# Kernel tuning notes

Hardware: AMD Instinct MI355X
Metric: run time of the kernel (lower is better)

Reference implementation:

```python
import jax, jax.numpy as jnp
import numpy as np

B, T, C = 4, 2048, 768
H, D = 12, 64          # num_heads, head_size
R = 64                 # kv_lora_rank
ROPE_THETA = 10000.0


def setup_inputs() -> dict:
    key = jax.random.key(0)
    ks = jax.random.split(key, 8)
    s = lambda fan_in: 1.0 / np.sqrt(fan_in)
    return {
        "x":      jax.random.normal(ks[0], (B, T, C), jnp.float32),
        "Wq":     jax.random.normal(ks[1], (C, H * D), jnp.float32) * s(C),
        "Wdown":  jax.random.normal(ks[2], (C, R), jnp.float32) * s(C),
        "ln_g":   jnp.ones((R,), jnp.float32),
        "ln_b":   jnp.zeros((R,), jnp.float32),
        "Wup":    jax.random.normal(ks[3], (R, 2 * H * D), jnp.float32) * s(R),
        "Wo":     jax.random.normal(ks[4], (H * D, C), jnp.float32) * s(H * D),
        "bo":     jnp.zeros((C,), jnp.float32),
    }


def _rope_cos_sin(t, d, dtype):
    # freqs over half-dim, repeated twice (rotate-half convention)
    inv_freq = 1.0 / (ROPE_THETA ** (jnp.arange(0, d, 2, dtype=jnp.float32) / d))
    ang = jnp.arange(t, dtype=jnp.float32)[:, None] * inv_freq[None, :]  # [T, D/2]
    ang = jnp.concatenate([ang, ang], axis=-1)                            # [T, D]
    return jnp.cos(ang).astype(dtype), jnp.sin(ang).astype(dtype)


def _apply_rope(q, cos, sin):
    # q: [B, H, T, D]; cos/sin: [T, D]
    d2 = q.shape[-1] // 2
    rot = jnp.concatenate([-q[..., d2:], q[..., :d2]], axis=-1)
    return q * cos + rot * sin


def reference(x, Wq, Wdown, ln_g, ln_b, Wup, Wo, bo):
    b, t, c = x.shape
    q = (x @ Wq).reshape(b, t, H, D).transpose(0, 2, 1, 3)  # [B,H,T,D]

    ckv = x @ Wdown                                         # [B,T,R]
    mu = jnp.mean(ckv, axis=-1, keepdims=True)
    var = jnp.var(ckv, axis=-1, keepdims=True)
    ckv = (ckv - mu) * jax.lax.rsqrt(var + 1e-5) * ln_g + ln_b

    kv = (ckv @ Wup).reshape(b, t, 2, H, D)
    k = kv[:, :, 0].transpose(0, 2, 1, 3)                   # [B,H,T,D]
    v = kv[:, :, 1].transpose(0, 2, 1, 3)

    cos, sin = _rope_cos_sin(t, D, x.dtype)
    q = _apply_rope(q, cos, sin)
    k = _apply_rope(k, cos, sin)

    wei = jnp.einsum("bhqd,bhkd->bhqk", q, k) * (D ** -0.5)
    causal = jnp.tril(jnp.ones((t, t), bool))
    wei = jnp.where(causal, wei, -jnp.inf)
    wei = jax.nn.softmax(wei, axis=-1)                      # dropout: eval mode (identity)

    out = jnp.einsum("bhqk,bhkd->bhqd", wei, v)             # [B,H,T,D]
    out = out.transpose(0, 2, 1, 3).reshape(b, t, H * D)
    return out @ Wo + bo
```

## Files before the change

kernel.cpp:

```cpp
#include <hip/hip_runtime.h>
#include <hip/hip_bf16.h>
#include <math.h>

#define B_ 4
#define T_ 2048
#define C_ 768
#define H_ 12
#define D_ 64
#define R_ 64
#define BT_ (B_*T_)
#define HD_ (H_*D_)

typedef __attribute__((ext_vector_type(8))) short bf16x8;
typedef __attribute__((ext_vector_type(4))) float f32x4;

__device__ inline short f2bf(float f) {
  union { float f; unsigned u; } x; x.f = f;
  unsigned r = x.u + 0x7fffu + ((x.u >> 16) & 1u);
  return (short)(r >> 16);
}
__device__ inline float bf2f(short s) {
  union { unsigned u; float f; } x; x.u = ((unsigned)(unsigned short)s) << 16;
  return x.f;
}
__device__ inline unsigned pk_bf16(float a, float b) {
#if __has_builtin(__builtin_amdgcn_cvt_pk_bf16_f32)
  auto t = __builtin_amdgcn_cvt_pk_bf16_f32(a, b);
  unsigned u; __builtin_memcpy(&u, &t, sizeof(unsigned)); return u;
#else
  union { float f; unsigned u; } x, y; x.f = a; y.f = b;
  unsigned ra = (x.u + 0x7fffu + ((x.u >> 16) & 1u)) >> 16;
  unsigned rb = (y.u + 0x7fffu + ((y.u >> 16) & 1u)) & 0xffff0000u;
  return ra | rb;
#endif
}
__device__ inline float fexp2(float x) {
#if __has_builtin(__builtin_amdgcn_exp2f)
  return __builtin_amdgcn_exp2f(x);
#else
  return exp2f(x);
#endif
}
typedef __attribute__((address_space(3))) unsigned lds_u32;
typedef __attribute__((address_space(1))) const unsigned glb_u32;
__device__ inline void gload_lds16(const void* g, void* l) {
  __builtin_amdgcn_global_load_lds((glb_u32*)g, (lds_u32*)l, 16, 0, 0);
}

__global__ void convert_f32_bf16(const float* __restrict__ in, short* __restrict__ out, int n4) {
  int i = blockIdx.x * blockDim.x + threadIdx.x;
  if (i < n4) {
    float4 v = ((const float4*)in)[i];
    short4 o;
    o.x = f2bf(v.x); o.y = f2bf(v.y); o.z = f2bf(v.z); o.w = f2bf(v.w);
    ((short4*)out)[i] = o;
  }
}

__global__ void prep_all(const float* __restrict__ Wq, const float* __restrict__ Wd,
                         const float* __restrict__ Wup, const float* __restrict__ Wo,
                         short* __restrict__ W1T, short* __restrict__ WupT,
                         short* __restrict__ WoT,
                         float* __restrict__ cs, float* __restrict__ sn) {
  int idx = blockIdx.x * blockDim.x + threadIdx.x;
  const int S1 = 768*768, S2 = 64*768, S3 = 1536*64, S4 = 768*768, S5 = T_*32;
  if (idx < S1) {
    int n = idx / 768, k = idx - n*768;
    W1T[idx] = f2bf(Wq[(size_t)k*768 + n]);
  } else if (idx < S1+S2) {
    int i = idx - S1; int n = i / 768, k = i - n*768;
    W1T[idx] = f2bf(Wd[(size_t)k*64 + n]);
  } else if (idx < S1+S2+S3) {
    int i = idx - S1 - S2; int n = i / 64, k = i - n*64;
    WupT[i] = f2bf(Wup[(size_t)k*1536 + n]);
  } else if (idx < S1+S2+S3+S4) {
    int i = idx - S1 - S2 - S3; int n = i / 768, k = i - n*768;
    WoT[i] = f2bf(Wo[(size_t)k*768 + n]);
  } else if (idx < S1+S2+S3+S4+S5) {
    int i = idx - S1 - S2 - S3 - S4;
    int j = i & 31, t = i >> 5;
    float invf = exp2f(-(float)j * (13.287712379549449f / 32.f));
    float a = (float)t * invf;
    cs[i] = cosf(a);
    sn[i] = sinf(a);
  }
}

template<int MODE>
__global__ __launch_bounds__(256) void gemm128(
    const short* __restrict__ A, const short* __restrict__ Bt,
    int M, int N, int K, int NBvalid,
    float* __restrict__ out0, const float* __restrict__ bias,
    const float* __restrict__ bias2,
    short* __restrict__ ob0, short* __restrict__ ob1,
    const float* __restrict__ cs, const float* __restrict__ sn)
{
  __shared__ short As[128 * 64];
  __shared__ short Bs[128 * 64];
  const int m0 = blockIdx.x * 128;
  const int n0 = blockIdx.y * 128;
  const int tid = threadIdx.x, lane = tid & 63, w = tid >> 6;
  const int wr = w >> 1, wc = w & 1;
  const int fr = lane & 15, fk = (lane >> 4) * 8;
  const int rstage = lane >> 3;
  const int cstage = (lane & 7) * 8;

  f32x4 acc[4][4] = {};

  for (int k0 = 0; k0 < K; k0 += 64) {
    __syncthreads();
    #pragma unroll
    for (int i = 0; i < 4; ++i) {
      int c = w * 4 + i;
      int r = c * 8 + rstage;
      gload_lds16(&A[(size_t)(m0 + r) * K + k0 + cstage], &As[c * 512]);
      if (n0 + c * 8 < NBvalid)
        gload_lds16(&Bt[(size_t)(n0 + r) * K + k0 + cstage], &Bs[c * 512]);
    }
    __syncthreads();
    #pragma unroll
    for (int kk = 0; kk < 64; kk += 32) {
      bf16x8 a[4], b[4];
      #pragma unroll
      for (int i = 0; i < 4; ++i) {
        a[i] = *(const bf16x8*)&As[(wr * 64 + i * 16 + fr) * 64 + kk + fk];
        b[i] = *(const bf16x8*)&Bs[(wc * 64 + i * 16 + fr) * 64 + kk + fk];
      }
      #pragma unroll
      for (int mi = 0; mi < 4; ++mi)
        #pragma unroll
        for (int ni = 0; ni < 4; ++ni)
          acc[mi][ni] = __builtin_amdgcn_mfma_f32_16x16x32_bf16(a[mi], b[ni], acc[mi][ni], 0, 0, 0);
    }
  }

  const int er = (lane >> 4) * 4, ec = lane & 15;
  const int colbase = n0 + wc * 64;

  if constexpr (MODE == 2) {
    #pragma unroll
    for (int mi = 0; mi < 4; ++mi)
      #pragma unroll
      for (int r = 0; r < 4; ++r) {
        int row = m0 + wr * 64 + mi * 16 + er + r;
        #pragma unroll
        for (int ni = 0; ni < 4; ++ni) {
          int col = colbase + ni * 16 + ec;
          out0[(size_t)row * N + col] = acc[mi][ni][r] + bias[col];
        }
      }
    return;
  }

  if constexpr (MODE == 0) {
    if (colbase < 768) {
      int h = colbase >> 6;
      #pragma unroll
      for (int mi = 0; mi < 4; ++mi)
        #pragma unroll
        for (int r = 0; r < 4; ++r) {
          int row = m0 + wr * 64 + mi * 16 + er + r;
          int t = row & (T_ - 1), bb = row >> 11;
          short* dst = ob0 + (((size_t)(bb * H_ + h)) * T_ + t) * 64;
          #pragma unroll
          for (int ni = 0; ni < 2; ++ni) {
            int d = ni * 16 + ec;
            float c = cs[t * 32 + d], s = sn[t * 32 + d];
            float x0 = acc[mi][ni][r], x1 = acc[mi][ni + 2][r];
            dst[d]      = f2bf(x0 * c - x1 * s);
            dst[d + 32] = f2bf(x1 * c + x0 * s);
          }
        }
    } else if (colbase < 832) {
      #pragma unroll
      for (int mi = 0; mi < 4; ++mi)
        #pragma unroll
        for (int r = 0; r < 4; ++r) {
          float s = 0.f, s2 = 0.f;
          #pragma unroll
          for (int ni = 0; ni < 4; ++ni) { float v = acc[mi][ni][r]; s += v; s2 += v*v; }
          #pragma unroll
          for (int off = 1; off < 16; off <<= 1) {
            s  += __shfl_xor(s, off);
            s2 += __shfl_xor(s2, off);
          }
          float mu = s * (1.f/64.f);
          float var = s2 * (1.f/64.f) - mu * mu;
          float rstd = rsqrtf(var + 1e-5f);
          int row = m0 + wr * 64 + mi * 16 + er + r;
          #pragma unroll
          for (int ni = 0; ni < 4; ++ni) {
            int d = ni * 16 + ec;
            ob1[(size_t)row * 64 + d] = f2bf((acc[mi][ni][r] - mu) * rstd * bias[d] + bias2[d]);
          }
        }
    }
  } else {
    if (colbase < 768) {
      int h = colbase >> 6;
      #pragma unroll
      for (int mi = 0; mi < 4; ++mi)
        #pragma unroll
        for (int r = 0; r < 4; ++r) {
          int row = m0 + wr * 64 + mi * 16 + er + r;
          int t = row & (T_ - 1), bb = row >> 11;
          short* dst = ob0 + (((size_t)(bb * H_ + h)) * T_ + t) * 64;
          #pragma unroll
          for (int ni = 0; ni < 2; ++ni) {
            int d = ni * 16 + ec;
            float c = cs[t * 32 + d], s = sn[t * 32 + d];
            float x0 = acc[mi][ni][r], x1 = acc[mi][ni + 2][r];
            dst[d]      = f2bf(x0 * c - x1 * s);
            dst[d + 32] = f2bf(x1 * c + x0 * s);
          }
        }
    } else {
      __syncthreads();
      short* Wl = (w < 2) ? &As[w * 4096] : &Bs[(w - 2) * 4096];
      int h = (colbase - 768) >> 6;
      #pragma unroll
      for (int mi = 0; mi < 4; ++mi) {
        int tl0 = mi * 16 + er;
        #pragma unroll
        for (int ni = 0; ni < 4; ++ni) {
          int d = ni * 16 + ec;
          int col = (tl0 + (d & 7) * 8) & 63;
          uint2 uu;
          uu.x = pk_bf16(acc[mi][ni][0], acc[mi][ni][1]);
          uu.y = pk_bf16(acc[mi][ni][2], acc[mi][ni][3]);
          *(uint2*)&Wl[d * 64 + col] = uu;
        }
      }
      __syncthreads();
      int bb = m0 >> 11;
      int tg0 = (m0 & (T_ - 1)) + wr * 64;
      int dlow = lane >> 3, tc = lane & 7;
      #pragma unroll
      for (int j = 0; j < 8; ++j) {
        int d = j * 8 + dlow;
        int col = (tc * 8 + (d & 7) * 8) & 63;
        uint4 vv = *(const uint4*)&Wl[d * 64 + col];
        *(uint4*)&ob1[((size_t)(bb * H_ + h) * 64 + d) * T_ + tg0 + tc * 8] = vv;
      }
    }
  }
}

#define SC2_ 0.18033688f

__global__ __launch_bounds__(256) void attn_mfma(
    const short* __restrict__ qgl, const short* __restrict__ kg,
    const short* __restrict__ vtg, short* __restrict__ o)
{
  __shared__ short Ks[8 * 512];
  __shared__ short Vts[8 * 512];
  __shared__ short Ps[4 * 16 * 72];

  const int bh = blockIdx.x;
  const int tid = threadIdx.x, lane = tid & 63, w = tid >> 6;
  const int q16 = lane & 15, quad = lane >> 4;
  short* Pw = &Ps[w * 16 * 72];
  const short* kb  = kg  + (size_t)bh * T_ * 64;
  const short* vtb = vtg + (size_t)bh * 64 * T_;
  const int b = bh / H_, h = bh - b * H_;

  #pragma unroll
  for (int phase = 0; phase < 2; ++phase) {
    const int qt = phase == 0 ? (31 - (int)blockIdx.y) : (int)blockIdx.y;
    const int q0 = qt * 64 + w * 16;
    const int qidx = q0 + q16;

    const short* qrow = qgl + ((size_t)bh * T_ + qidx) * 64;
    bf16x8 bq0 = *(const bf16x8*)&qrow[quad * 8];
    bf16x8 bq1 = *(const bf16x8*)&qrow[32 + quad * 8];

    f32x4 oacc[4] = {};
    float lrun = 0.f;
    const int qlast = qt * 64;

    for (int kt = 0; kt <= qlast; kt += 64) {
      __syncthreads();
      #pragma unroll
      for (int i = 0; i < 2; ++i) {
        int c = w * 2 + i;
        int s = c >> 1, ch = c & 1;
        gload_lds16(kb  + (size_t)(kt + s * 16 + q16) * 64 + ch * 32 + quad * 8, &Ks[c * 512]);
        gload_lds16(vtb + (size_t)(s * 16 + q16) * T_ + kt + ch * 32 + quad * 8, &Vts[c * 512]);
      }
      __syncthreads();

      f32x4 sacc[4];
      #pragma unroll
      for (int s = 0; s < 4; ++s) {
        bf16x8 a0 = *(const bf16x8*)&Ks[(s * 2 + 0) * 512 + lane * 8];
        bf16x8 a1 = *(const bf16x8*)&Ks[(s * 2 + 1) * 512 + lane * 8];
        f32x4 t0 = {};
        t0 = __builtin_amdgcn_mfma_f32_16x16x32_bf16(a0, bq0, t0, 0, 0, 0);
        t0 = __builtin_amdgcn_mfma_f32_16x16x32_bf16(a1, bq1, t0, 0, 0, 0);
        sacc[s] = t0;
      }

      float pv[16];
      float ls = 0.f;
      if (kt != qlast) {
        #pragma unroll
        for (int s = 0; s < 4; ++s)
          #pragma unroll
          for (int r = 0; r < 4; ++r) {
            float p = fexp2(sacc[s][r] * SC2_);
            pv[s * 4 + r] = p; ls += p;
          }
      } else {
        #pragma unroll
        for (int s = 0; s < 4; ++s)
          #pragma unroll
          for (int r = 0; r < 4; ++r) {
            int key = kt + s * 16 + quad * 4 + r;
            float p = (key <= qidx) ? fexp2(sacc[s][r] * SC2_) : 0.f;
            pv[s * 4 + r] = p; ls += p;
          }
      }
      ls += __shfl_xor(ls, 16);
      ls += __shfl_xor(ls, 32);
      lrun += ls;

      #pragma unroll
      for (int s = 0; s < 4; ++s) {
        uint2 uu;
        uu.x = pk_bf16(pv[s * 4 + 0], pv[s * 4 + 1]);
        uu.y = pk_bf16(pv[s * 4 + 2], pv[s * 4 + 3]);
        *(uint2*)&Pw[q16 * 72 + s * 16 + quad * 4] = uu;
      }

      #pragma unroll
      for (int c = 0; c < 2; ++c) {
        bf16x8 bp = *(const bf16x8*)&Pw[q16 * 72 + c * 32 + quad * 8];
        #pragma unroll
        for (int ms = 0; ms < 4; ++ms) {
          bf16x8 av = *(const bf16x8*)&Vts[(ms * 2 + c) * 512 + lane * 8];
          oacc[ms] = __builtin_amdgcn_mfma_f32_16x16x32_bf16(av, bp, oacc[ms], 0, 0, 0);
        }
      }
    }

    float inv = 1.f / lrun;
    #pragma unroll
    for (int ms = 0; ms < 4; ++ms) {
      uint2 uu;
      uu.x = pk_bf16(oacc[ms][0] * inv, oacc[ms][1] * inv);
      uu.y = pk_bf16(oacc[ms][2] * inv, oacc[ms][3] * inv);
      *(uint2*)&Pw[q16 * 72 + ms * 16 + quad * 4] = uu;
    }
    int row = lane >> 2, cc2 = (lane & 3) * 16;
    uint4 r0 = *(const uint4*)&Pw[row * 72 + cc2];
    uint4 r1 = *(const uint4*)&Pw[row * 72 + cc2 + 8];
    int t = q0 + row;
    short* orow = o + ((size_t)(b * T_ + t)) * HD_ + h * 64 + cc2;
    *(uint4*)&orow[0] = r0;
    *(uint4*)&orow[8] = r1;
  }
}

extern "C" void kernel_launch(void* const* d_in, const int* in_sizes, int n_in,
                              void* d_out, int out_size, void* d_ws, size_t ws_size,
                              hipStream_t stream) {
  (void)in_sizes; (void)n_in; (void)out_size; (void)ws_size;
  const float* x     = (const float*)d_in[0];
  const float* Wq    = (const float*)d_in[1];
  const float* Wdown = (const float*)d_in[2];
  const float* ln_g  = (const float*)d_in[3];
  const float* ln_b  = (const float*)d_in[4];
  const float* Wup   = (const float*)d_in[5];
  const float* Wo    = (const float*)d_in[6];
  const float* bo    = (const float*)d_in[7];
  float* out = (float*)d_out;

  char* w = (char*)d_ws;
  short* x_bf   = (short*)w;  w += (size_t)BT_ * C_    * 2;
  short* W1T    = (short*)w;  w += (size_t)832 * C_    * 2;
  short* WupT   = (short*)w;  w += (size_t)2*HD_ * R_  * 2;
  short* WoT    = (short*)w;  w += (size_t)HD_ * C_    * 2;
  short* ckv    = (short*)w;  w += (size_t)BT_ * R_    * 2;
  short* qb     = (short*)w;  w += (size_t)BT_ * HD_   * 2;
  short* kb     = (short*)w;  w += (size_t)BT_ * HD_   * 2;
  short* vt     = (short*)w;  w += (size_t)BT_ * HD_   * 2;
  short* att    = (short*)w;  w += (size_t)BT_ * HD_   * 2;
  float* cs_t   = (float*)w;  w += (size_t)T_ * 32 * 4;
  float* sn_t   = (float*)w;  w += (size_t)T_ * 32 * 4;

  {
    const int tot = 768*768 + 64*768 + 1536*64 + 768*768 + T_*32;
    prep_all<<<(tot + 255)/256, 256, 0, stream>>>(Wq, Wdown, Wup, Wo, W1T, WupT, WoT, cs_t, sn_t);
  }
  convert_f32_bf16<<<(BT_*C_/4 + 255)/256, 256, 0, stream>>>(x, x_bf, BT_*C_/4);

  gemm128<0><<<dim3(BT_/128, 7), 256, 0, stream>>>(
      x_bf, W1T, BT_, 896, C_, 832, nullptr, ln_g, ln_b, qb, ckv, cs_t, sn_t);

  gemm128<1><<<dim3(BT_/128, 12), 256, 0, stream>>>(
      ckv, WupT, BT_, 2*HD_, R_, 2*HD_, nullptr, nullptr, nullptr, kb, vt, cs_t, sn_t);

  attn_mfma<<<dim3(B_*H_, 16), 256, 0, stream>>>(qb, kb, vt, att);

  gemm128<2><<<dim3(BT_/128, 6), 256, 0, stream>>>(
      att, WoT, BT_, C_, HD_, C_, out, bo, nullptr, nullptr, nullptr, nullptr, nullptr);
}
```

Baseline: 207.2 us.

## Share K/V tiles across paired query tiles with double-buffered loads; tile weight transposes

The attention kernel now processes both paired query tiles (long and short causal rows) in one pass over the key tiles. Each K/V tile is loaded once and reused for both, and the next tile is prefetched into a second LDS buffer while the current one is computed. The softmax scale is folded into the RoPE cos/sin applied to q, which removes a multiply per score. The weight-prep kernel now transposes through a padded shared-memory tile so global reads and writes are coalesced. The costs are doubled LDS for K/V and more accumulator registers, which may reduce occupancy.

```diff
diff --git a/kernel.cpp b/kernel.cpp
--- a/kernel.cpp
+++ b/kernel.cpp
@@ -57,34 +57,52 @@
   }
 }
 
-__global__ void prep_all(const float* __restrict__ Wq, const float* __restrict__ Wd,
-                         const float* __restrict__ Wup, const float* __restrict__ Wo,
-                         short* __restrict__ W1T, short* __restrict__ WupT,
-                         short* __restrict__ WoT,
-                         float* __restrict__ cs, float* __restrict__ sn) {
-  int idx = blockIdx.x * blockDim.x + threadIdx.x;
-  const int S1 = 768*768, S2 = 64*768, S3 = 1536*64, S4 = 768*768, S5 = T_*32;
-  if (idx < S1) {
-    int n = idx / 768, k = idx - n*768;
-    W1T[idx] = f2bf(Wq[(size_t)k*768 + n]);
-  } else if (idx < S1+S2) {
-    int i = idx - S1; int n = i / 768, k = i - n*768;
-    W1T[idx] = f2bf(Wd[(size_t)k*64 + n]);
-  } else if (idx < S1+S2+S3) {
-    int i = idx - S1 - S2; int n = i / 64, k = i - n*64;
-    WupT[i] = f2bf(Wup[(size_t)k*1536 + n]);
-  } else if (idx < S1+S2+S3+S4) {
-    int i = idx - S1 - S2 - S3; int n = i / 768, k = i - n*768;
-    WoT[i] = f2bf(Wo[(size_t)k*768 + n]);
-  } else if (idx < S1+S2+S3+S4+S5) {
-    int i = idx - S1 - S2 - S3 - S4;
-    int j = i & 31, t = i >> 5;
-    float invf = exp2f(-(float)j * (13.287712379549449f / 32.f));
-    float a = (float)t * invf;
-    cs[i] = cosf(a);
-    sn[i] = sinf(a);
-  }
-}
+__device__ inline void ttile(const float* __restrict__ src, short* __restrict__ dst,
+                             int K, int N, int k0, int n0, int tid, float (*tl)[33]) {
+  int tx = tid & 31, ty = tid >> 5;
+  #pragma unroll
+  for (int r = 0; r < 4; ++r)
+    tl[ty + 8 * r][tx] = src[(size_t)(k0 + ty + 8 * r) * N + n0 + tx];
+  __syncthreads();
+  #pragma unroll
+  for (int r = 0; r < 4; ++r)
+    dst[(size_t)(n0 + ty + 8 * r) * K + k0 + tx] = f2bf(tl[tx][ty + 8 * r]);
+}
+
+__global__ __launch_bounds__(256) void prep_all(
+    const float* __restrict__ Wq, const float* __restrict__ Wd,
+    const float* __restrict__ Wup, const float* __restrict__ Wo,
+    short* __restrict__ W1T, short* __restrict__ WupT, short* __restrict__ WoT,
+    float* __restrict__ cs, float* __restrict__ sn) {
+  __shared__ float tl[32][33];
+  int blk = blockIdx.x, tid = threadIdx.x;
+  if (blk < 576) {
+    int tk = blk % 24, tn = blk / 24;
+    ttile(Wq, W1T, 768, 768, tk * 32, tn * 32, tid, tl);
+  } else if (blk < 624) {
+    int l = blk - 576; int tk = l % 24, tn = l / 24;
+    ttile(Wd, W1T + (size_t)768 * 768, 768, 64, tk * 32, tn * 32, tid, tl);
+  } else if (blk < 720) {
+    int l = blk - 624; int tk = l % 2, tn = l / 2;
+    ttile(Wup, WupT, 64, 1536, tk * 32, tn * 32, tid, tl);
+  } else if (blk < 1296) {
+    int l = blk - 720; int tk = l % 24, tn = l / 24;
+    ttile(Wo, WoT, 768, 768, tk * 32, tn * 32, tid, tl);
+  } else {
+    int base = (blk - 1296) * 1024;
+    #pragma unroll
+    for (int i = 0; i < 4; ++i) {
+      int idx = base + tid + i * 256;
+      int j = idx & 31, t = idx >> 5;
+      float invf = exp2f(-(float)j * (13.287712379549449f / 32.f));
+      float a = (float)t * invf;
+      cs[idx] = cosf(a);
+      sn[idx] = sinf(a);
+    }
+  }
+}
+
+#define SC2_ 0.18033688f
 
 template<int MODE>
 __global__ __launch_bounds__(256) void gemm128(
@@ -165,7 +183,7 @@
           #pragma unroll
           for (int ni = 0; ni < 2; ++ni) {
             int d = ni * 16 + ec;
-            float c = cs[t * 32 + d], s = sn[t * 32 + d];
+            float c = cs[t * 32 + d] * SC2_, s = sn[t * 32 + d] * SC2_;
             float x0 = acc[mi][ni][r], x1 = acc[mi][ni + 2][r];
             dst[d]      = f2bf(x0 * c - x1 * s);
             dst[d + 32] = f2bf(x1 * c + x0 * s);
@@ -246,17 +264,17 @@
   }
 }
 
-#define SC2_ 0.18033688f
-
 __global__ __launch_bounds__(256) void attn_mfma(
     const short* __restrict__ qgl, const short* __restrict__ kg,
     const short* __restrict__ vtg, short* __restrict__ o)
 {
-  __shared__ short Ks[8 * 512];
-  __shared__ short Vts[8 * 512];
+  __shared__ short Ks[2][4096];
+  __shared__ short Vts[2][4096];
   __shared__ short Ps[4 * 16 * 72];
 
   const int bh = blockIdx.x;
+  const int y  = blockIdx.y;
+  const int qt1 = 31 - y, qt2 = y;
   const int tid = threadIdx.x, lane = tid & 63, w = tid >> 6;
   const int q16 = lane & 15, quad = lane >> 4;
   short* Pw = &Ps[w * 16 * 72];
@@ -264,50 +282,61 @@
   const short* vtb = vtg + (size_t)bh * 64 * T_;
   const int b = bh / H_, h = bh - b * H_;
 
+  const int qbase[2] = {qt1 * 64 + w * 16, qt2 * 64 + w * 16};
+  bf16x8 bq[2][2];
   #pragma unroll
-  for (int phase = 0; phase < 2; ++phase) {
-    const int qt = phase == 0 ? (31 - (int)blockIdx.y) : (int)blockIdx.y;
-    const int q0 = qt * 64 + w * 16;
-    const int qidx = q0 + q16;
-
-    const short* qrow = qgl + ((size_t)bh * T_ + qidx) * 64;
-    bf16x8 bq0 = *(const bf16x8*)&qrow[quad * 8];
-    bf16x8 bq1 = *(const bf16x8*)&qrow[32 + quad * 8];
-
-    f32x4 oacc[4] = {};
-    float lrun = 0.f;
-    const int qlast = qt * 64;
-
-    for (int kt = 0; kt <= qlast; kt += 64) {
-      __syncthreads();
-      #pragma unroll
-      for (int i = 0; i < 2; ++i) {
-        int c = w * 2 + i;
-        int s = c >> 1, ch = c & 1;
-        gload_lds16(kb  + (size_t)(kt + s * 16 + q16) * 64 + ch * 32 + quad * 8, &Ks[c * 512]);
-        gload_lds16(vtb + (size_t)(s * 16 + q16) * T_ + kt + ch * 32 + quad * 8, &Vts[c * 512]);
-      }
-      __syncthreads();
+  for (int g = 0; g < 2; ++g) {
+    const short* qrow = qgl + ((size_t)bh * T_ + qbase[g] + q16) * 64;
+    bq[g][0] = *(const bf16x8*)&qrow[quad * 8];
+    bq[g][1] = *(const bf16x8*)&qrow[32 + quad * 8];
+  }
+
+  f32x4 oacc[2][4] = {};
+  float lrun[2] = {0.f, 0.f};
+  const int last  = qt1 * 64;
+  const int last2 = qt2 * 64;
+
+  auto stage = [&](int kt, int ib) {
+    #pragma unroll
+    for (int i = 0; i < 2; ++i) {
+      int c = w * 2 + i;
+      int s = c >> 1, ch = c & 1;
+      gload_lds16(kb  + (size_t)(kt + s * 16 + q16) * 64 + ch * 32 + quad * 8, &Ks[ib][c * 512]);
+      gload_lds16(vtb + (size_t)(s * 16 + q16) * T_ + kt + ch * 32 + quad * 8, &Vts[ib][c * 512]);
+    }
+  };
+
+  stage(0, 0);
+  int ib = 0;
+  for (int kt = 0; kt <= last; kt += 64, ib ^= 1) {
+    __syncthreads();
+    if (kt + 64 <= last) stage(kt + 64, ib ^ 1);
+
+    #pragma unroll
+    for (int g = 0; g < 2; ++g) {
+      if (g == 1 && kt > last2) break;
+      const int diag_end = (g == 0) ? last : last2;
+      const int qidx = qbase[g] + q16;
 
       f32x4 sacc[4];
       #pragma unroll
       for (int s = 0; s < 4; ++s) {
-        bf16x8 a0 = *(const bf16x8*)&Ks[(s * 2 + 0) * 512 + lane * 8];
-        bf16x8 a1 = *(const bf16x8*)&Ks[(s * 2 + 1) * 512 + lane * 8];
+        bf16x8 a0 = *(const bf16x8*)&Ks[ib][(s * 2 + 0) * 512 + lane * 8];
+        bf16x8 a1 = *(const bf16x8*)&Ks[ib][(s * 2 + 1) * 512 + lane * 8];
         f32x4 t0 = {};
-        t0 = __builtin_amdgcn_mfma_f32_16x16x32_bf16(a0, bq0, t0, 0, 0, 0);
-        t0 = __builtin_amdgcn_mfma_f32_16x16x32_bf16(a1, bq1, t0, 0, 0, 0);
+        t0 = __builtin_amdgcn_mfma_f32_16x16x32_bf16(a0, bq[g][0], t0, 0, 0, 0);
+        t0 = __builtin_amdgcn_mfma_f32_16x16x32_bf16(a1, bq[g][1], t0, 0, 0, 0);
         sacc[s] = t0;
       }
 
       float pv[16];
       float ls = 0.f;
-      if (kt != qlast) {
+      if (kt != diag_end) {
         #pragma unroll
         for (int s = 0; s < 4; ++s)
           #pragma unroll
           for (int r = 0; r < 4; ++r) {
-            float p = fexp2(sacc[s][r] * SC2_);
+            float p = fexp2(sacc[s][r]);
             pv[s * 4 + r] = p; ls += p;
           }
       } else {
@@ -316,13 +345,13 @@
           #pragma unroll
           for (int r = 0; r < 4; ++r) {
             int key = kt + s * 16 + quad * 4 + r;
-            float p = (key <= qidx) ? fexp2(sacc[s][r] * SC2_) : 0.f;
+            float p = (key <= qidx) ? fexp2(sacc[s][r]) : 0.f;
             pv[s * 4 + r] = p; ls += p;
           }
       }
       ls += __shfl_xor(ls, 16);
       ls += __shfl_xor(ls, 32);
-      lrun += ls;
+      lrun[g] += ls;
 
       #pragma unroll
       for (int s = 0; s < 4; ++s) {
@@ -337,24 +366,27 @@
         bf16x8 bp = *(const bf16x8*)&Pw[q16 * 72 + c * 32 + quad * 8];
         #pragma unroll
         for (int ms = 0; ms < 4; ++ms) {
-          bf16x8 av = *(const bf16x8*)&Vts[(ms * 2 + c) * 512 + lane * 8];
-          oacc[ms] = __builtin_amdgcn_mfma_f32_16x16x32_bf16(av, bp, oacc[ms], 0, 0, 0);
-        }
-      }
-    }
-
-    float inv = 1.f / lrun;
+          bf16x8 av = *(const bf16x8*)&Vts[ib][(ms * 2 + c) * 512 + lane * 8];
+          oacc[g][ms] = __builtin_amdgcn_mfma_f32_16x16x32_bf16(av, bp, oacc[g][ms], 0, 0, 0);
+        }
+      }
+    }
+  }
+
+  #pragma unroll
+  for (int g = 0; g < 2; ++g) {
+    float inv = 1.f / lrun[g];
     #pragma unroll
     for (int ms = 0; ms < 4; ++ms) {
       uint2 uu;
-      uu.x = pk_bf16(oacc[ms][0] * inv, oacc[ms][1] * inv);
-      uu.y = pk_bf16(oacc[ms][2] * inv, oacc[ms][3] * inv);
+      uu.x = pk_bf16(oacc[g][ms][0] * inv, oacc[g][ms][1] * inv);
+      uu.y = pk_bf16(oacc[g][ms][2] * inv, oacc[g][ms][3] * inv);
       *(uint2*)&Pw[q16 * 72 + ms * 16 + quad * 4] = uu;
     }
     int row = lane >> 2, cc2 = (lane & 3) * 16;
     uint4 r0 = *(const uint4*)&Pw[row * 72 + cc2];
     uint4 r1 = *(const uint4*)&Pw[row * 72 + cc2 + 8];
-    int t = q0 + row;
+    int t = qbase[g] + row;
     short* orow = o + ((size_t)(b * T_ + t)) * HD_ + h * 64 + cc2;
     *(uint4*)&orow[0] = r0;
     *(uint4*)&orow[8] = r1;
@@ -388,10 +420,7 @@
   float* cs_t   = (float*)w;  w += (size_t)T_ * 32 * 4;
   float* sn_t   = (float*)w;  w += (size_t)T_ * 32 * 4;
 
-  {
-    const int tot = 768*768 + 64*768 + 1536*64 + 768*768 + T_*32;
-    prep_all<<<(tot + 255)/256, 256, 0, stream>>>(Wq, Wdown, Wup, Wo, W1T, WupT, WoT, cs_t, sn_t);
-  }
+  prep_all<<<1360, 256, 0, stream>>>(Wq, Wdown, Wup, Wo, W1T, WupT, WoT, cs_t, sn_t);
   convert_f32_bf16<<<(BT_*C_/4 + 255)/256, 256, 0, stream>>>(x, x_bf, BT_*C_/4);
 
   gemm128<0><<<dim3(BT_/128, 7), 256, 0, stream>>>(
```

New measurement: 222.8 us. +7.5%, slower.
